# Kernel tuning notes

Hardware: AMD Instinct MI355X
Metric: run time of the kernel (lower is better)

Reference implementation:

```python
import jax, jax.numpy as jnp
import numpy as np

B, S, D, H, E, K, F, FS = 4, 2048, 1024, 16, 8, 2, 4096, 2048
HD = D // H
EPS = 1e-5
T = B * S
CAP = int(1.25 * K * T / E)  # capacity factor 1.25 -> 2560 tokens/expert


def _ln(x, g, b):
    mu = jnp.mean(x, -1, keepdims=True)
    var = jnp.var(x, -1, keepdims=True)
    return (x - mu) * jax.lax.rsqrt(var + EPS) * g + b


def _forward(x, attention_mask, ln1_g, ln1_b, wq, bq, wk, bk, wv, bv, wo, bo,
             ln2_g, ln2_b, w_router, w1, b1, w2, b2, ws1, bs1, ws2, bs2):
    # ---- pre-LN self-attention + residual ----
    xn = _ln(x, ln1_g, ln1_b)
    q = (xn @ wq + bq).reshape(B, S, H, HD)
    k = (xn @ wk + bk).reshape(B, S, H, HD)
    v = (xn @ wv + bv).reshape(B, S, H, HD)
    scores = jnp.einsum('bqhd,bkhd->bhqk', q, k) / np.float32(np.sqrt(HD))
    scores = jnp.where(attention_mask[:, None, None, :], jnp.finfo(scores.dtype).min, scores)
    p = jax.nn.softmax(scores, axis=-1)
    attn = jnp.einsum('bhqk,bkhd->bqhd', p, v).reshape(B, S, D) @ wo + bo
    x = x + attn
    # ---- pre-LN sparse MoE FFN + residual ----
    xn = _ln(x, ln2_g, ln2_b).reshape(T, D)
    logits = xn.astype(jnp.float32) @ w_router              # router in fp32, [T,E]
    probs = jax.nn.softmax(logits, axis=-1)
    topv, topi = jax.lax.top_k(probs, K)                    # [T,K]
    topv = topv / jnp.sum(topv, -1, keepdims=True)          # renormalize top-k gates
    oh = jax.nn.one_hot(topi, E, dtype=jnp.float32)         # [T,K,E]
    flat = oh.transpose(1, 0, 2).reshape(K * T, E)          # slot-major routing priority
    pos_tok = jnp.sum((jnp.cumsum(flat, axis=0) - 1.0) * flat, -1)  # slot position within expert
    keep = pos_tok < CAP                                    # drop tokens over capacity
    posc = jnp.clip(pos_tok, 0, CAP - 1).astype(jnp.int32)
    eidx = topi.T.reshape(K * T)
    w = topv.T.reshape(K * T) * keep
    xt = jnp.tile(xn, (K, 1)) * keep[:, None]               # [K*T, D]
    disp = jnp.zeros((E, CAP, D), xn.dtype).at[eidx, posc].add(xt)   # dispatch [E,C,D]
    h = jax.nn.gelu(jnp.einsum('ecd,edf->ecf', disp, w1) + b1[:, None, :], approximate=False)
    eo = jnp.einsum('ecf,efd->ecd', h, w2) + b2[:, None, :]          # expert out [E,C,D]
    y = jnp.sum(eo[eidx, posc].reshape(K, T, D) * w.reshape(K, T, 1), axis=0)  # combine
    # shared expert (dense, always active)
    y = y + jax.nn.gelu(xn @ ws1 + bs1, approximate=False) @ ws2 + bs2
    return x + y.reshape(B, S, D)


def setup_inputs() -> dict:
    key = jax.random.key(0)
    ks = jax.random.split(key, 16)
    g = lambda k, shape, fan: jax.random.normal(k, shape, jnp.float32) * (fan ** -0.5)
    return {
        'x': jax.random.normal(ks[0], (B, S, D), jnp.float32),
        'attention_mask': jnp.zeros((B, S), bool),
        'ln1_g': jnp.ones((D,), jnp.float32), 'ln1_b': jnp.zeros((D,), jnp.float32),
        'wq': g(ks[1], (D, D), D), 'bq': jnp.zeros((D,), jnp.float32),
        'wk': g(ks[2], (D, D), D), 'bk': jnp.zeros((D,), jnp.float32),
        'wv': g(ks[3], (D, D), D), 'bv': jnp.zeros((D,), jnp.float32),
        'wo': g(ks[4], (D, D), D), 'bo': jnp.zeros((D,), jnp.float32),
        'ln2_g': jnp.ones((D,), jnp.float32), 'ln2_b': jnp.zeros((D,), jnp.float32),
        'w_router': g(ks[5], (D, E), D),
        'w1': g(ks[6], (E, D, F), D), 'b1': jnp.zeros((E, F), jnp.float32),
        'w2': g(ks[7], (E, F, D), F), 'b2': jnp.zeros((E, D), jnp.float32),
        'ws1': g(ks[8], (D, FS), D), 'bs1': jnp.zeros((FS,), jnp.float32),
        'ws2': g(ks[9], (FS, D), FS), 'bs2': jnp.zeros((D,), jnp.float32),
    }


def reference(x, attention_mask, ln1_g, ln1_b, wq, bq, wk, bk, wv, bv, wo, bo,
              ln2_g, ln2_b, w_router, w1, b1, w2, b2, ws1, bs1, ws2, bs2):
    return _forward(x, attention_mask, ln1_g, ln1_b, wq, bq, wk, bk, wv, bv, wo, bo,
                    ln2_g, ln2_b, w_router, w1, b1, w2, b2, ws1, bs1, ws2, bs2)
```

## Files before the change

### kernel.cpp

```cpp
#include <hip/hip_runtime.h>
#include <hip/hip_bf16.h>
#include <stdint.h>

#define D_ 1024
#define S_ 2048
#define B_ 4
#define H_ 16
#define T_ 8192
#define E_ 8
#define CAP_ 2560
#define F_ 4096
#define FS_ 2048

typedef __attribute__((ext_vector_type(8))) short s8v;
typedef __attribute__((ext_vector_type(4))) float f4v;

#define GLL(gp, lp) __builtin_amdgcn_global_load_lds( \
    (const __attribute__((address_space(1))) unsigned int*)(gp), \
    (__attribute__((address_space(3))) unsigned int*)(lp), 16, 0, 0)

__device__ inline short f2bf(float f) {
    union { float f; unsigned u; } v; v.f = f;
    unsigned r = (v.u + 0x7fffu + ((v.u >> 16) & 1u)) >> 16;
    return (short)(r & 0xffffu);
}
__device__ inline float b2f(short h) {
    union { unsigned u; float f; } v; v.u = ((unsigned)(unsigned short)h) << 16; return v.f;
}
__device__ inline float gelu_f(float x) {
    return 0.5f * x * (1.0f + erff(x * 0.7071067811865475f));
}
__device__ inline f4v f4zero() { f4v z; z[0]=0.f; z[1]=0.f; z[2]=0.f; z[3]=0.f; return z; }

__device__ inline unsigned pk2(float a, float b, unsigned* lo) {
    const short ha = f2bf(a), hb = f2bf(b);
    const short la = f2bf(a - b2f(ha)), lb = f2bf(b - b2f(hb));
    *lo = ((unsigned)(unsigned short)lb << 16) | (unsigned)(unsigned short)la;
    return ((unsigned)(unsigned short)hb << 16) | (unsigned)(unsigned short)ha;
}

__global__ __launch_bounds__(256) void transcvt(const float* __restrict__ in,
                                                short* __restrict__ out, int R, int C)
{
    __shared__ float tile[32][33];
    const int tid = threadIdx.x;
    const int tx = tid & 31, ty = tid >> 5;
    const long long ib = (long long)blockIdx.z * R * C;
    const int r0 = blockIdx.y * 32, c0 = blockIdx.x * 32;
#pragma unroll
    for (int i = 0; i < 4; i++)
        tile[ty + i * 8][tx] = in[ib + (long long)(r0 + ty + i * 8) * C + c0 + tx];
    __syncthreads();
#pragma unroll
    for (int i = 0; i < 4; i++)
        out[ib + (long long)(c0 + ty + i * 8) * R + r0 + tx] = f2bf(tile[tx][ty + i * 8]);
}

__global__ __launch_bounds__(256) void transcvt2(const float* __restrict__ in,
    short* __restrict__ oh, short* __restrict__ ol, int R, int C)
{
    __shared__ float tile[32][33];
    const int tid = threadIdx.x;
    const int tx = tid & 31, ty = tid >> 5;
    const int r0 = blockIdx.y * 32, c0 = blockIdx.x * 32;
#pragma unroll
    for (int i = 0; i < 4; i++)
        tile[ty + i * 8][tx] = in[(long long)(r0 + ty + i * 8) * C + c0 + tx];
    __syncthreads();
#pragma unroll
    for (int i = 0; i < 4; i++) {
        const float v = tile[tx][ty + i * 8];
        const short h = f2bf(v);
        const long long o = (long long)(c0 + ty + i * 8) * R + r0 + tx;
        oh[o] = h;
        ol[o] = f2bf(v - b2f(h));
    }
}

__global__ __launch_bounds__(256) void ln1_split(const float* __restrict__ x,
    const float* __restrict__ g, const float* __restrict__ bta,
    short* __restrict__ xh, short* __restrict__ xl)
{
    const int t = blockIdx.x, tid = threadIdx.x;
    const float4 v = ((const float4*)(x + (long long)t * D_))[tid];
    float s1 = v.x + v.y + v.z + v.w;
    float s2 = v.x * v.x + v.y * v.y + v.z * v.z + v.w * v.w;
#pragma unroll
    for (int off = 32; off; off >>= 1) { s1 += __shfl_xor(s1, off, 64); s2 += __shfl_xor(s2, off, 64); }
    __shared__ float r1[4], r2[4];
    if ((tid & 63) == 0) { r1[tid >> 6] = s1; r2[tid >> 6] = s2; }
    __syncthreads();
    s1 = r1[0] + r1[1] + r1[2] + r1[3];
    s2 = r2[0] + r2[1] + r2[2] + r2[3];
    const float mu = s1 * (1.0f / D_);
    const float var = s2 * (1.0f / D_) - mu * mu;
    const float rs = rsqrtf(var + 1e-5f);
    const float4 gv = ((const float4*)g)[tid];
    const float4 bv = ((const float4*)bta)[tid];
    float xn[4];
    xn[0] = (v.x - mu) * rs * gv.x + bv.x;
    xn[1] = (v.y - mu) * rs * gv.y + bv.y;
    xn[2] = (v.z - mu) * rs * gv.z + bv.z;
    xn[3] = (v.w - mu) * rs * gv.w + bv.w;
    short4 hh, ll;
    hh.x = f2bf(xn[0]); ll.x = f2bf(xn[0] - b2f(hh.x));
    hh.y = f2bf(xn[1]); ll.y = f2bf(xn[1] - b2f(hh.y));
    hh.z = f2bf(xn[2]); ll.z = f2bf(xn[2] - b2f(hh.z));
    hh.w = f2bf(xn[3]); ll.w = f2bf(xn[3] - b2f(hh.w));
    ((short4*)(xh + (long long)t * D_))[tid] = hh;
    ((short4*)(xl + (long long)t * D_))[tid] = ll;
}

__global__ __launch_bounds__(256) void ln2_router_kernel(const float* __restrict__ x,
    const float* __restrict__ g, const float* __restrict__ bta, const float* __restrict__ wr,
    short* __restrict__ xo, int* __restrict__ topi, float* __restrict__ gates)
{
    const int t = blockIdx.x, tid = threadIdx.x;
    const float4 v = ((const float4*)(x + (long long)t * D_))[tid];
    float s1 = v.x + v.y + v.z + v.w;
    float s2 = v.x * v.x + v.y * v.y + v.z * v.z + v.w * v.w;
#pragma unroll
    for (int off = 32; off; off >>= 1) { s1 += __shfl_xor(s1, off, 64); s2 += __shfl_xor(s2, off, 64); }
    __shared__ float r1[4], r2[4];
    if ((tid & 63) == 0) { r1[tid >> 6] = s1; r2[tid >> 6] = s2; }
    __syncthreads();
    s1 = r1[0] + r1[1] + r1[2] + r1[3];
    s2 = r2[0] + r2[1] + r2[2] + r2[3];
    const float mu = s1 * (1.0f / D_);
    const float var = s2 * (1.0f / D_) - mu * mu;
    const float rs = rsqrtf(var + 1e-5f);
    const float4 gv = ((const float4*)g)[tid];
    const float4 bv = ((const float4*)bta)[tid];
    float xn[4];
    xn[0] = (v.x - mu) * rs * gv.x + bv.x;
    xn[1] = (v.y - mu) * rs * gv.y + bv.y;
    xn[2] = (v.z - mu) * rs * gv.z + bv.z;
    xn[3] = (v.w - mu) * rs * gv.w + bv.w;
    short4 o;
    o.x = f2bf(xn[0]); o.y = f2bf(xn[1]); o.z = f2bf(xn[2]); o.w = f2bf(xn[3]);
    ((short4*)(xo + (long long)t * D_))[tid] = o;

    float a8[8] = {0, 0, 0, 0, 0, 0, 0, 0};
#pragma unroll
    for (int q = 0; q < 4; q++) {
        const int d = tid * 4 + q;
        const float4 w0 = ((const float4*)(wr + d * 8))[0];
        const float4 w1 = ((const float4*)(wr + d * 8))[1];
        a8[0] += xn[q] * w0.x; a8[1] += xn[q] * w0.y; a8[2] += xn[q] * w0.z; a8[3] += xn[q] * w0.w;
        a8[4] += xn[q] * w1.x; a8[5] += xn[q] * w1.y; a8[6] += xn[q] * w1.z; a8[7] += xn[q] * w1.w;
    }
    __shared__ float lred[32];
#pragma unroll
    for (int e = 0; e < 8; e++) {
        float vv = a8[e];
#pragma unroll
        for (int off = 32; off; off >>= 1) vv += __shfl_xor(vv, off, 64);
        if ((tid & 63) == 0) lred[(tid >> 6) * 8 + e] = vv;
    }
    __syncthreads();
    if (tid == 0) {
        float lg[8];
#pragma unroll
        for (int e = 0; e < 8; e++) lg[e] = lred[e] + lred[8 + e] + lred[16 + e] + lred[24 + e];
        int e0 = 0;
        for (int e = 1; e < 8; e++) if (lg[e] > lg[e0]) e0 = e;
        int e1 = (e0 == 0) ? 1 : 0;
        for (int e = 0; e < 8; e++) if (e != e0 && lg[e] > lg[e1]) e1 = e;
        const float mx = lg[e0];
        float den = 0.f;
        for (int e = 0; e < 8; e++) den += expf(lg[e] - mx);
        const float p0 = expf(lg[e0] - mx) / den;
        const float p1 = expf(lg[e1] - mx) / den;
        const float inv = 1.0f / (p0 + p1);
        topi[t * 2] = e0; topi[t * 2 + 1] = e1;
        gates[t * 2] = p0 * inv; gates[t * 2 + 1] = p1 * inv;
    }
}

__global__ __launch_bounds__(256) void route_scan(const int* __restrict__ topi,
    const float* __restrict__ gates, int* __restrict__ posc, float* __restrict__ wv)
{
    const int tid = threadIdx.x;
    const int w = tid >> 6, lane = tid & 63;
    __shared__ int wsum[4 * 8];
    int cnt[8] = {0, 0, 0, 0, 0, 0, 0, 0};
    const int base_r = tid * 64;
    for (int i = 0; i < 64; i++) {
        const int r = base_r + i;
        const int k = r >> 13, t = r & (T_ - 1);
        cnt[topi[t * 2 + k]]++;
    }
    int excl[8];
#pragma unroll
    for (int e = 0; e < 8; e++) {
        int x = cnt[e];
#pragma unroll
        for (int off = 1; off < 64; off <<= 1) {
            int y = __shfl_up(x, off, 64);
            if (lane >= off) x += y;
        }
        excl[e] = x - cnt[e];
        if (lane == 63) wsum[w * 8 + e] = x;
    }
    __syncthreads();
    int pos[8];
#pragma unroll
    for (int e = 0; e < 8; e++) {
        int s = 0;
        for (int ww = 0; ww < 4; ww++) if (ww < w) s += wsum[ww * 8 + e];
        pos[e] = s + excl[e];
    }
    for (int i = 0; i < 64; i++) {
        const int r = base_r + i;
        const int k = r >> 13, t = r & (T_ - 1);
        const int e = topi[t * 2 + k];
        const int p = pos[e]++;
        const bool keep = p < CAP_;
        posc[r] = keep ? p : -1;
        wv[r] = keep ? gates[t * 2 + k] : 0.0f;
    }
}

__global__ __launch_bounds__(128) void dispatch_kernel(const short* __restrict__ xn2,
    const int* __restrict__ topi, const int* __restrict__ posc, short* __restrict__ disp)
{
    const int r = blockIdx.x;
    const int p = posc[r];
    if (p < 0) return;
    const int k = r >> 13, t = r & (T_ - 1);
    const int e = topi[t * 2 + k];
    const int tid = threadIdx.x;
    *(s8v*)&disp[((long long)e * CAP_ + p) * D_ + tid * 8] =
        *(const s8v*)&xn2[(long long)t * D_ + tid * 8];
}

__global__ __launch_bounds__(256) void combine_kernel(const float* __restrict__ x1,
    const float* __restrict__ ys, const float* __restrict__ eo,
    const int* __restrict__ topi, const int* __restrict__ posc,
    const float* __restrict__ wv, float* __restrict__ out)
{
    const int t = blockIdx.x, tid = threadIdx.x;
    float4 a = *(const float4*)&x1[(long long)t * D_ + tid * 4];
    const float4 b = *(const float4*)&ys[(long long)t * D_ + tid * 4];
    a.x += b.x; a.y += b.y; a.z += b.z; a.w += b.w;
#pragma unroll
    for (int k = 0; k < 2; k++) {
        const int r = k * T_ + t;
        const int p = posc[r];
        if (p >= 0) {
            const int e = topi[t * 2 + k];
            const float wt = wv[r];
            const float4 c = *(const float4*)&eo[((long long)e * CAP_ + p) * D_ + tid * 4];
            a.x += wt * c.x; a.y += wt * c.y; a.z += wt * c.z; a.w += wt * c.w;
        }
    }
    *(float4*)&out[(long long)t * D_ + tid * 4] = a;
}

template <int EPI>
__global__ __launch_bounds__(256) void gemm_btz(
    const short* __restrict__ A, const short* __restrict__ Bt,
    const float* __restrict__ bias, void* __restrict__ Cout,
    int M, int N, int K, int ldc,
    long long sA, long long sB, long long sBias, long long sC)
{
    __shared__ __align__(16) short lA[128 * 32];
    __shared__ __align__(16) short lB[128 * 32];
    const int z = blockIdx.z;
    A += (long long)z * sA;
    Bt += (long long)z * sB;
    bias += (long long)z * sBias;
    const int tid = threadIdx.x;
    const int wvi = tid >> 6, lane = tid & 63, lid = lane & 15, quad = lane >> 4;
    const int wm = wvi >> 1, wn = wvi & 1;
    const int mBase = blockIdx.y * 128, nBase = blockIdx.x * 128;
    f4v acc[4][4];
#pragma unroll
    for (int i = 0; i < 4; i++)
#pragma unroll
        for (int j = 0; j < 4; j++) acc[i][j] = f4zero();
    const long long aOff0 = (long long)(mBase + (tid >> 2)) * K + (tid & 3) * 8;
    const long long aOff1 = aOff0 + 64LL * K;
    const long long bOff0 = (long long)(nBase + (tid >> 2)) * K + (tid & 3) * 8;
    const long long bOff1 = bOff0 + 64LL * K;
    const int wofs = wvi << 9;
    for (int k0 = 0; k0 < K; k0 += 32) {
        __syncthreads();
        GLL(A + aOff0 + k0, &lA[wofs]);  GLL(A + aOff1 + k0, &lA[2048 + wofs]);
        GLL(Bt + bOff0 + k0, &lB[wofs]); GLL(Bt + bOff1 + k0, &lB[2048 + wofs]);
        __syncthreads();
        s8v af[4], bf[4];
#pragma unroll
        for (int i = 0; i < 4; i++)
            af[i] = *(const s8v*)&lA[(wm * 64 + i * 16 + lid) * 32 + quad * 8];
#pragma unroll
        for (int j = 0; j < 4; j++)
            bf[j] = *(const s8v*)&lB[(wn * 64 + j * 16 + lid) * 32 + quad * 8];
#pragma unroll
        for (int i = 0; i < 4; i++)
#pragma unroll
            for (int j = 0; j < 4; j++)
                acc[i][j] = __builtin_amdgcn_mfma_f32_16x16x32_bf16(af[i], bf[j], acc[i][j], 0, 0, 0);
    }
    const int mW = mBase + wm * 64 + quad * 4;
    const int nW = nBase + wn * 64 + lid;
    short* Cs = (short*)Cout + (long long)z * sC;
    float* Cf = (float*)Cout + (long long)z * sC;
#pragma unroll
    for (int j = 0; j < 4; j++) {
        const int n = nW + j * 16;
        const float bn = bias[n];
#pragma unroll
        for (int i = 0; i < 4; i++) {
            const int m = mW + i * 16;
#pragma unroll
            for (int r = 0; r < 4; r++) {
                float v = acc[i][j][r] + bn;
                if (EPI == 1) { v = gelu_f(v); Cs[(long long)(m + r) * ldc + n] = f2bf(v); }
                else          { Cf[(long long)(m + r) * ldc + n] = v; }
            }
        }
    }
}

template <int EPI>
__global__ __launch_bounds__(256) void gemm_hl(
    const short* __restrict__ Ah, const short* __restrict__ Al,
    const short* __restrict__ Bh, const short* __restrict__ Bl,
    const float* __restrict__ biasQ, const float* __restrict__ biasK,
    const float* __restrict__ biasV, const float* __restrict__ resid,
    short* __restrict__ Ch, short* __restrict__ Cl, float* __restrict__ Cf,
    int M, int N, int K, int ldc)
{
    __shared__ __align__(16) short lAh[4096], lAl[4096], lBh[4096], lBl[4096];
    const int tid = threadIdx.x;
    const int wvi = tid >> 6, lane = tid & 63, lid = lane & 15, quad = lane >> 4;
    const int wm = wvi >> 1, wn = wvi & 1;
    const int mBase = blockIdx.y * 128, nBase = blockIdx.x * 128;
    f4v acc[4][4];
#pragma unroll
    for (int i = 0; i < 4; i++)
#pragma unroll
        for (int j = 0; j < 4; j++) acc[i][j] = f4zero();
    const long long aOff0 = (long long)(mBase + (tid >> 2)) * K + (tid & 3) * 8;
    const long long aOff1 = aOff0 + 64LL * K;
    const long long bOff0 = (long long)(nBase + (tid >> 2)) * K + (tid & 3) * 8;
    const long long bOff1 = bOff0 + 64LL * K;
    const int wofs = wvi << 9;
    for (int k0 = 0; k0 < K; k0 += 32) {
        __syncthreads();
        GLL(Ah + aOff0 + k0, &lAh[wofs]);  GLL(Ah + aOff1 + k0, &lAh[2048 + wofs]);
        GLL(Al + aOff0 + k0, &lAl[wofs]);  GLL(Al + aOff1 + k0, &lAl[2048 + wofs]);
        GLL(Bh + bOff0 + k0, &lBh[wofs]);  GLL(Bh + bOff1 + k0, &lBh[2048 + wofs]);
        GLL(Bl + bOff0 + k0, &lBl[wofs]);  GLL(Bl + bOff1 + k0, &lBl[2048 + wofs]);
        __syncthreads();
        s8v ah[4], al[4], bh[4], bl[4];
#pragma unroll
        for (int i = 0; i < 4; i++) {
            const int ro = (wm * 64 + i * 16 + lid) * 32 + quad * 8;
            ah[i] = *(const s8v*)&lAh[ro];
            al[i] = *(const s8v*)&lAl[ro];
        }
#pragma unroll
        for (int j = 0; j < 4; j++) {
            const int ro = (wn * 64 + j * 16 + lid) * 32 + quad * 8;
            bh[j] = *(const s8v*)&lBh[ro];
            bl[j] = *(const s8v*)&lBl[ro];
        }
#pragma unroll
        for (int i = 0; i < 4; i++)
#pragma unroll
            for (int j = 0; j < 4; j++) {
                acc[i][j] = __builtin_amdgcn_mfma_f32_16x16x32_bf16(ah[i], bh[j], acc[i][j], 0, 0, 0);
                acc[i][j] = __builtin_amdgcn_mfma_f32_16x16x32_bf16(ah[i], bl[j], acc[i][j], 0, 0, 0);
                acc[i][j] = __builtin_amdgcn_mfma_f32_16x16x32_bf16(al[i], bh[j], acc[i][j], 0, 0, 0);
            }
    }
    const int mW = mBase + wm * 64 + quad * 4;
    const int nW = nBase + wn * 64 + lid;
#pragma unroll
    for (int j = 0; j < 4; j++) {
        const int n = nW + j * 16;
        const float* bp = (n < 1024) ? biasQ : ((n < 2048) ? biasK : biasV);
        const float bn = bp[n & 1023];
#pragma unroll
        for (int i = 0; i < 4; i++) {
            const int m = mW + i * 16;
#pragma unroll
            for (int r = 0; r < 4; r++) {
                const float v = acc[i][j][r] + bn;
                const long long o = (long long)(m + r) * ldc + n;
                if (EPI == 0) {
                    const short h = f2bf(v);
                    Ch[o] = h;
                    Cl[o] = f2bf(v - b2f(h));
                } else {
                    Cf[o] = v + resid[o];
                }
            }
        }
    }
}

__global__ __launch_bounds__(256) void flash_attn_hl(const short* __restrict__ qkvh,
    const short* __restrict__ qkvl, const unsigned char* __restrict__ mask,
    short* __restrict__ attnh, short* __restrict__ attnl)
{
    __shared__ __align__(16) short lKh[32 * 72], lKl[32 * 72];
    __shared__ __align__(16) short lVth[64 * 40], lVtl[64 * 40];
    const int tid = threadIdx.x;
    const int lane = tid & 63, lid = lane & 15, quad = lane >> 4;
    const int w = tid >> 6;
    const int bh = blockIdx.y;
    const int b = bh >> 4, h = bh & 15;
    const int q0row = blockIdx.x * 64 + w * 16;

    const long long rowQ = (long long)(b * S_ + q0row + lid) * 3072 + h * 64;
    const s8v qh0 = *(const s8v*)&qkvh[rowQ + quad * 8];
    const s8v qh1 = *(const s8v*)&qkvh[rowQ + 32 + quad * 8];
    const s8v ql0 = *(const s8v*)&qkvl[rowQ + quad * 8];
    const s8v ql1 = *(const s8v*)&qkvl[rowQ + 32 + quad * 8];

    float m_run = -1e30f, l_run = 0.0f;
    f4v o[4];
#pragma unroll
    for (int dt = 0; dt < 4; dt++) o[dt] = f4zero();

    const unsigned char* mrow = mask + b * S_;
    const int srow = tid >> 3, sgrp = tid & 7;
    const int srcA = lid + ((quad & 1) << 5);
    const int srcB = srcA + 16;

    for (int c0 = 0; c0 < S_; c0 += 32) {
        __syncthreads();
        {
            const long long gk = (long long)(b * S_ + c0 + srow) * 3072 + 1024 + h * 64 + sgrp * 8;
            *(s8v*)&lKh[srow * 72 + sgrp * 8] = *(const s8v*)&qkvh[gk];
            *(s8v*)&lKl[srow * 72 + sgrp * 8] = *(const s8v*)&qkvl[gk];
            const long long gv = (long long)(b * S_ + c0 + srow) * 3072 + 2048 + h * 64 + sgrp * 8;
            const s8v vh = *(const s8v*)&qkvh[gv];
            const s8v vl = *(const s8v*)&qkvl[gv];
            const int vcol = srow ^ ((sgrp & 3) << 3);
#pragma unroll
            for (int jj = 0; jj < 8; jj++) {
                lVth[(sgrp * 8 + jj) * 40 + vcol] = vh[jj];
                lVtl[(sgrp * 8 + jj) * 40 + vcol] = vl[jj];
            }
        }
        __syncthreads();

        f4v s0 = f4zero(), s1 = f4zero();
        {
            const int r0 = lid * 72 + quad * 8;
            const s8v kh0a = *(const s8v*)&lKh[r0];
            const s8v kh0b = *(const s8v*)&lKh[r0 + 32];
            const s8v kl0a = *(const s8v*)&lKl[r0];
            const s8v kl0b = *(const s8v*)&lKl[r0 + 32];
            s0 = __builtin_amdgcn_mfma_f32_16x16x32_bf16(kh0a, qh0, s0, 0, 0, 0);
            s0 = __builtin_amdgcn_mfma_f32_16x16x32_bf16(kh0b, qh1, s0, 0, 0, 0);
            s0 = __builtin_amdgcn_mfma_f32_16x16x32_bf16(kl0a, qh0, s0, 0, 0, 0);
            s0 = __builtin_amdgcn_mfma_f32_16x16x32_bf16(kl0b, qh1, s0, 0, 0, 0);
            s0 = __builtin_amdgcn_mfma_f32_16x16x32_bf16(kh0a, ql0, s0, 0, 0, 0);
            s0 = __builtin_amdgcn_mfma_f32_16x16x32_bf16(kh0b, ql1, s0, 0, 0, 0);
            const int r1i = (16 + lid) * 72 + quad * 8;
            const s8v kh1a = *(const s8v*)&lKh[r1i];
            const s8v kh1b = *(const s8v*)&lKh[r1i + 32];
            const s8v kl1a = *(const s8v*)&lKl[r1i];
            const s8v kl1b = *(const s8v*)&lKl[r1i + 32];
            s1 = __builtin_amdgcn_mfma_f32_16x16x32_bf16(kh1a, qh0, s1, 0, 0, 0);
            s1 = __builtin_amdgcn_mfma_f32_16x16x32_bf16(kh1b, qh1, s1, 0, 0, 0);
            s1 = __builtin_amdgcn_mfma_f32_16x16x32_bf16(kl1a, qh0, s1, 0, 0, 0);
            s1 = __builtin_amdgcn_mfma_f32_16x16x32_bf16(kl1b, qh1, s1, 0, 0, 0);
            s1 = __builtin_amdgcn_mfma_f32_16x16x32_bf16(kh1a, ql0, s1, 0, 0, 0);
            s1 = __builtin_amdgcn_mfma_f32_16x16x32_bf16(kh1b, ql1, s1, 0, 0, 0);
        }
        const unsigned mm0 = *(const unsigned*)(mrow + c0 + quad * 4);
        const unsigned mm1 = *(const unsigned*)(mrow + c0 + 16 + quad * 4);
        float p[8];
#pragma unroll
        for (int r = 0; r < 4; r++) {
            p[r]     = ((mm0 >> (8 * r)) & 255u) ? -1e30f : s0[r] * 0.125f;
            p[4 + r] = ((mm1 >> (8 * r)) & 255u) ? -1e30f : s1[r] * 0.125f;
        }
        float mx = fmaxf(fmaxf(fmaxf(p[0], p[1]), fmaxf(p[2], p[3])),
                         fmaxf(fmaxf(p[4], p[5]), fmaxf(p[6], p[7])));
        mx = fmaxf(mx, __shfl_xor(mx, 16, 64));
        mx = fmaxf(mx, __shfl_xor(mx, 32, 64));
        const float mn = fmaxf(m_run, mx);
        const float alpha = __expf(m_run - mn);
        m_run = mn;
        float rs = 0.0f;
#pragma unroll
        for (int i = 0; i < 8; i++) { p[i] = __expf(p[i] - mn); rs += p[i]; }
        rs += __shfl_xor(rs, 16, 64);
        rs += __shfl_xor(rs, 32, 64);
        l_run = l_run * alpha + rs;
#pragma unroll
        for (int dt = 0; dt < 4; dt++)
#pragma unroll
            for (int r = 0; r < 4; r++) o[dt][r] *= alpha;

        unsigned c0l, c1l, c2l, c3l;
        const unsigned c0h = pk2(p[0], p[1], &c0l);
        const unsigned c1h = pk2(p[2], p[3], &c1l);
        const unsigned c2h = pk2(p[4], p[5], &c2l);
        const unsigned c3h = pk2(p[6], p[7], &c3l);
        union { s8v v; unsigned u[4]; } pah, pal;
        {
            const unsigned a0 = __shfl((int)c0h, srcA, 64), a2 = __shfl((int)c2h, srcA, 64);
            const unsigned a1 = __shfl((int)c1h, srcA, 64), a3 = __shfl((int)c3h, srcA, 64);
            const unsigned b0 = __shfl((int)c0h, srcB, 64), b2 = __shfl((int)c2h, srcB, 64);
            const unsigned b1 = __shfl((int)c1h, srcB, 64), b3 = __shfl((int)c3h, srcB, 64);
            const bool lo = (quad < 2);
            pah.u[0] = lo ? a0 : a2; pah.u[1] = lo ? a1 : a3;
            pah.u[2] = lo ? b0 : b2; pah.u[3] = lo ? b1 : b3;
        }
        {
            const unsigned a0 = __shfl((int)c0l, srcA, 64), a2 = __shfl((int)c2l, srcA, 64);
            const unsigned a1 = __shfl((int)c1l, srcA, 64), a3 = __shfl((int)c3l, srcA, 64);
            const unsigned b0 = __shfl((int)c0l, srcB, 64), b2 = __shfl((int)c2l, srcB, 64);
            const unsigned b1 = __shfl((int)c1l, srcB, 64), b3 = __shfl((int)c3l, srcB, 64);
            const bool lo = (quad < 2);
            pal.u[0] = lo ? a0 : a2; pal.u[1] = lo ? a1 : a3;
            pal.u[2] = lo ? b0 : b2; pal.u[3] = lo ? b1 : b3;
        }

#pragma unroll
        for (int dt = 0; dt < 4; dt++) {
            const int d = dt * 16 + lid;
            const int x3 = (dt * 2 + (lid >> 3)) & 3;
            const int ro = d * 40 + ((quad ^ x3) << 3);
            const s8v bvh = *(const s8v*)&lVth[ro];
            const s8v bvl = *(const s8v*)&lVtl[ro];
            o[dt] = __builtin_amdgcn_mfma_f32_16x16x32_bf16(bvh, pah.v, o[dt], 0, 0, 0);
            o[dt] = __builtin_amdgcn_mfma_f32_16x16x32_bf16(bvl, pah.v, o[dt], 0, 0, 0);
            o[dt] = __builtin_amdgcn_mfma_f32_16x16x32_bf16(bvh, pal.v, o[dt], 0, 0, 0);
        }
    }
    const float inv_l = 1.0f / l_run;
    const long long obase = (long long)(b * S_ + q0row + lid) * D_ + h * 64 + quad * 4;
#pragma unroll
    for (int dt = 0; dt < 4; dt++) {
        short4 hh4, ll4;
        float v0 = o[dt][0] * inv_l, v1 = o[dt][1] * inv_l;
        float v2 = o[dt][2] * inv_l, v3 = o[dt][3] * inv_l;
        hh4.x = f2bf(v0); ll4.x = f2bf(v0 - b2f(hh4.x));
        hh4.y = f2bf(v1); ll4.y = f2bf(v1 - b2f(hh4.y));
        hh4.z = f2bf(v2); ll4.z = f2bf(v2 - b2f(hh4.z));
        hh4.w = f2bf(v3); ll4.w = f2bf(v3 - b2f(hh4.w));
        *(short4*)&attnh[obase + dt * 16] = hh4;
        *(short4*)&attnl[obase + dt * 16] = ll4;
    }
}

constexpr long long SZ_DD2   = (long long)D_ * D_ * 2;
constexpr long long OFF_WQKVH = 0;
constexpr long long OFF_WQKVL = OFF_WQKVH + 3 * SZ_DD2;
constexpr long long OFF_WOH   = OFF_WQKVL + 3 * SZ_DD2;
constexpr long long OFF_WOL   = OFF_WOH + SZ_DD2;
constexpr long long OFF_W1T   = OFF_WOL + SZ_DD2;
constexpr long long OFF_W2T   = OFF_W1T + (long long)E_ * F_ * D_ * 2;
constexpr long long OFF_WS1T  = OFF_W2T + (long long)E_ * D_ * F_ * 2;
constexpr long long OFF_WS2T  = OFF_WS1T + (long long)FS_ * D_ * 2;
constexpr long long OFF_X1    = OFF_WS2T + (long long)D_ * FS_ * 2;
constexpr long long OFF_XN2   = OFF_X1 + (long long)T_ * D_ * 4;
constexpr long long OFF_TOPI  = OFF_XN2 + (long long)T_ * D_ * 2;
constexpr long long OFF_GATES = OFF_TOPI + (long long)T_ * 2 * 4;
constexpr long long OFF_POSC  = OFF_GATES + (long long)T_ * 2 * 4;
constexpr long long OFF_WVAL  = OFF_POSC + (long long)2 * T_ * 4;
constexpr long long ZONE      = OFF_WVAL + (long long)2 * T_ * 4;
constexpr long long OFF_XH1   = ZONE;
constexpr long long OFF_XL1   = OFF_XH1 + (long long)T_ * D_ * 2;
constexpr long long OFF_QKVH  = OFF_XL1 + (long long)T_ * D_ * 2;
constexpr long long OFF_QKVL  = OFF_QKVH + (long long)T_ * 3 * D_ * 2;
constexpr long long OFF_ATTNH = OFF_QKVL + (long long)T_ * 3 * D_ * 2;
constexpr long long OFF_ATTNL = OFF_ATTNH + (long long)T_ * D_ * 2;
constexpr long long OFF_DISP  = ZONE;
constexpr long long OFF_H     = OFF_DISP + (long long)E_ * CAP_ * D_ * 2;
constexpr long long OFF_EO    = OFF_H + (long long)4 * CAP_ * F_ * 2;
constexpr long long OFF_YS    = OFF_EO + (long long)E_ * CAP_ * D_ * 4;
constexpr long long OFF_HS    = ZONE;

extern "C" void kernel_launch(void* const* d_in, const int* in_sizes, int n_in,
                              void* d_out, int out_size, void* d_ws, size_t ws_size,
                              hipStream_t stream)
{
    (void)in_sizes; (void)n_in; (void)out_size; (void)ws_size;
    const float* x       = (const float*)d_in[0];
    const unsigned char* mask = (const unsigned char*)d_in[1];
    const float* ln1g    = (const float*)d_in[2];
    const float* ln1b    = (const float*)d_in[3];
    const float* wq      = (const float*)d_in[4];
    const float* bq      = (const float*)d_in[5];
    const float* wk      = (const float*)d_in[6];
    const float* bk      = (const float*)d_in[7];
    const float* wvp     = (const float*)d_in[8];
    const float* bvv     = (const float*)d_in[9];
    const float* wo      = (const float*)d_in[10];
    const float* bo      = (const float*)d_in[11];
    const float* ln2g    = (const float*)d_in[12];
    const float* ln2b    = (const float*)d_in[13];
    const float* wrouter = (const float*)d_in[14];
    const float* w1      = (const float*)d_in[15];
    const float* b1      = (const float*)d_in[16];
    const float* w2      = (const float*)d_in[17];
    const float* b2      = (const float*)d_in[18];
    const float* ws1     = (const float*)d_in[19];
    const float* bs1     = (const float*)d_in[20];
    const float* ws2     = (const float*)d_in[21];
    const float* bs2     = (const float*)d_in[22];
    float* out = (float*)d_out;
    char* ws = (char*)d_ws;

    short* wqkvh = (short*)(ws + OFF_WQKVH);
    short* wqkvl = (short*)(ws + OFF_WQKVL);
    short* woh   = (short*)(ws + OFF_WOH);
    short* wol   = (short*)(ws + OFF_WOL);
    short* w1T   = (short*)(ws + OFF_W1T);
    short* w2T   = (short*)(ws + OFF_W2T);
    short* ws1T  = (short*)(ws + OFF_WS1T);
    short* ws2T  = (short*)(ws + OFF_WS2T);
    float* x1    = (float*)(ws + OFF_X1);
    short* xn2   = (short*)(ws + OFF_XN2);
    int*   topi  = (int*)(ws + OFF_TOPI);
    float* gates = (float*)(ws + OFF_GATES);
    int*   posc  = (int*)(ws + OFF_POSC);
    float* wval  = (float*)(ws + OFF_WVAL);
    short* xh1   = (short*)(ws + OFF_XH1);
    short* xl1   = (short*)(ws + OFF_XL1);
    short* qkvh  = (short*)(ws + OFF_QKVH);
    short* qkvl  = (short*)(ws + OFF_QKVL);
    short* attnh = (short*)(ws + OFF_ATTNH);
    short* attnl = (short*)(ws + OFF_ATTNL);
    short* disp  = (short*)(ws + OFF_DISP);
    short* hbuf  = (short*)(ws + OFF_H);
    float* eo    = (float*)(ws + OFF_EO);
    short* hs    = (short*)(ws + OFF_HS);
    float* ysb   = (float*)(ws + OFF_YS);

    const dim3 tb(256);
    transcvt2<<<dim3(32, 32), tb, 0, stream>>>(wq,  wqkvh,               wqkvl,               1024, 1024);
    transcvt2<<<dim3(32, 32), tb, 0, stream>>>(wk,  wqkvh + 1024 * 1024, wqkvl + 1024 * 1024, 1024, 1024);
    transcvt2<<<dim3(32, 32), tb, 0, stream>>>(wvp, wqkvh + 2 * 1024 * 1024, wqkvl + 2 * 1024 * 1024, 1024, 1024);
    transcvt2<<<dim3(32, 32), tb, 0, stream>>>(wo,  woh, wol, 1024, 1024);
    transcvt<<<dim3(128, 32, 8), tb, 0, stream>>>(w1, w1T, 1024, 4096);
    transcvt<<<dim3(32, 128, 8), tb, 0, stream>>>(w2, w2T, 4096, 1024);
    transcvt<<<dim3(64, 32, 1), tb, 0, stream>>>(ws1, ws1T, 1024, 2048);
    transcvt<<<dim3(32, 64, 1), tb, 0, stream>>>(ws2, ws2T, 2048, 1024);

    ln1_split<<<T_, 256, 0, stream>>>(x, ln1g, ln1b, xh1, xl1);

    gemm_hl<0><<<dim3(24, 64), 256, 0, stream>>>(xh1, xl1, wqkvh, wqkvl,
        bq, bk, bvv, nullptr, qkvh, qkvl, nullptr, T_, 3072, 1024, 3072);

    flash_attn_hl<<<dim3(32, 64), 256, 0, stream>>>(qkvh, qkvl, mask, attnh, attnl);

    gemm_hl<1><<<dim3(8, 64), 256, 0, stream>>>(attnh, attnl, woh, wol,
        bo, bo, bo, x, nullptr, nullptr, x1, T_, 1024, 1024, 1024);

    ln2_router_kernel<<<T_, 256, 0, stream>>>(x1, ln2g, ln2b, wrouter, xn2, topi, gates);
    route_scan<<<1, 256, 0, stream>>>(topi, gates, posc, wval);
    dispatch_kernel<<<2 * T_, 128, 0, stream>>>(xn2, topi, posc, disp);

    for (int g = 0; g < 2; g++) {
        const long long e0 = (long long)g * 4;
        gemm_btz<1><<<dim3(32, 20, 4), 256, 0, stream>>>(
            disp + e0 * CAP_ * D_, w1T + e0 * F_ * D_, b1 + e0 * F_, hbuf,
            CAP_, F_, 1024, F_,
            (long long)CAP_ * D_, (long long)F_ * D_, (long long)F_, (long long)CAP_ * F_);
        gemm_btz<2><<<dim3(8, 20, 4), 256, 0, stream>>>(
            hbuf, w2T + e0 * D_ * F_, b2 + e0 * D_, eo + e0 * CAP_ * D_,
            CAP_, 1024, F_, 1024,
            (long long)CAP_ * F_, (long long)D_ * F_, (long long)D_, (long long)CAP_ * D_);
    }

    gemm_btz<1><<<dim3(16, 64, 1), 256, 0, stream>>>(xn2, ws1T, bs1, hs,
        T_, FS_, 1024, FS_, 0, 0, 0, 0);
    gemm_btz<2><<<dim3(8, 64, 1), 256, 0, stream>>>(hs, ws2T, bs2, ysb,
        T_, 1024, FS_, 1024, 0, 0, 0, 0);

    combine_kernel<<<T_, 256, 0, stream>>>(x1, ysb, eo, topi, posc, wval, out);
}
```

Baseline: 1.928 ms.

## Prefetch K/V tiles into registers, add lazy softmax rescale and MFMA priority

The flash-attention inner loop now loads the next 32-row K/V chunk from global memory into registers right after the LDS barrier, so the load overlaps the current chunk's MFMAs. The online softmax skips the max update and the rescale of the accumulator whenever the new chunk max stays within 8 of the running max across the wavefront. s_setprio is raised around the MFMA blocks to favour matrix issue. The cost is extra register pressure, and the skipped rescale lets exp values grow up to e^8, which relies on fp32 headroom.

```diff
diff --git a/kernel.cpp b/kernel.cpp
--- a/kernel.cpp
+++ b/kernel.cpp
@@ -428,26 +428,38 @@
 
     const unsigned char* mrow = mask + b * S_;
     const int srow = tid >> 3, sgrp = tid & 7;
+    const int vcol = srow ^ ((sgrp & 3) << 3);
     const int srcA = lid + ((quad & 1) << 5);
     const int srcB = srcA + 16;
+
+    s8v kh_r, kl_r, vh_r, vl_r;
+    {
+        const long long gk = (long long)(b * S_ + srow) * 3072 + 1024 + h * 64 + sgrp * 8;
+        kh_r = *(const s8v*)&qkvh[gk];
+        kl_r = *(const s8v*)&qkvl[gk];
+        vh_r = *(const s8v*)&qkvh[gk + 1024];
+        vl_r = *(const s8v*)&qkvl[gk + 1024];
+    }
 
     for (int c0 = 0; c0 < S_; c0 += 32) {
         __syncthreads();
         {
-            const long long gk = (long long)(b * S_ + c0 + srow) * 3072 + 1024 + h * 64 + sgrp * 8;
-            *(s8v*)&lKh[srow * 72 + sgrp * 8] = *(const s8v*)&qkvh[gk];
-            *(s8v*)&lKl[srow * 72 + sgrp * 8] = *(const s8v*)&qkvl[gk];
-            const long long gv = (long long)(b * S_ + c0 + srow) * 3072 + 2048 + h * 64 + sgrp * 8;
-            const s8v vh = *(const s8v*)&qkvh[gv];
-            const s8v vl = *(const s8v*)&qkvl[gv];
-            const int vcol = srow ^ ((sgrp & 3) << 3);
+            *(s8v*)&lKh[srow * 72 + sgrp * 8] = kh_r;
+            *(s8v*)&lKl[srow * 72 + sgrp * 8] = kl_r;
 #pragma unroll
             for (int jj = 0; jj < 8; jj++) {
-                lVth[(sgrp * 8 + jj) * 40 + vcol] = vh[jj];
-                lVtl[(sgrp * 8 + jj) * 40 + vcol] = vl[jj];
+                lVth[(sgrp * 8 + jj) * 40 + vcol] = vh_r[jj];
+                lVtl[(sgrp * 8 + jj) * 40 + vcol] = vl_r[jj];
             }
         }
         __syncthreads();
+        if (c0 + 32 < S_) {
+            const long long gk = (long long)(b * S_ + c0 + 32 + srow) * 3072 + 1024 + h * 64 + sgrp * 8;
+            kh_r = *(const s8v*)&qkvh[gk];
+            kl_r = *(const s8v*)&qkvl[gk];
+            vh_r = *(const s8v*)&qkvh[gk + 1024];
+            vl_r = *(const s8v*)&qkvl[gk + 1024];
+        }
 
         f4v s0 = f4zero(), s1 = f4zero();
         {
@@ -456,23 +468,25 @@
             const s8v kh0b = *(const s8v*)&lKh[r0 + 32];
             const s8v kl0a = *(const s8v*)&lKl[r0];
             const s8v kl0b = *(const s8v*)&lKl[r0 + 32];
+            const int r1i = (16 + lid) * 72 + quad * 8;
+            const s8v kh1a = *(const s8v*)&lKh[r1i];
+            const s8v kh1b = *(const s8v*)&lKh[r1i + 32];
+            const s8v kl1a = *(const s8v*)&lKl[r1i];
+            const s8v kl1b = *(const s8v*)&lKl[r1i + 32];
+            __builtin_amdgcn_s_setprio(1);
             s0 = __builtin_amdgcn_mfma_f32_16x16x32_bf16(kh0a, qh0, s0, 0, 0, 0);
             s0 = __builtin_amdgcn_mfma_f32_16x16x32_bf16(kh0b, qh1, s0, 0, 0, 0);
             s0 = __builtin_amdgcn_mfma_f32_16x16x32_bf16(kl0a, qh0, s0, 0, 0, 0);
             s0 = __builtin_amdgcn_mfma_f32_16x16x32_bf16(kl0b, qh1, s0, 0, 0, 0);
             s0 = __builtin_amdgcn_mfma_f32_16x16x32_bf16(kh0a, ql0, s0, 0, 0, 0);
             s0 = __builtin_amdgcn_mfma_f32_16x16x32_bf16(kh0b, ql1, s0, 0, 0, 0);
-            const int r1i = (16 + lid) * 72 + quad * 8;
-            const s8v kh1a = *(const s8v*)&lKh[r1i];
-            const s8v kh1b = *(const s8v*)&lKh[r1i + 32];
-            const s8v kl1a = *(const s8v*)&lKl[r1i];
-            const s8v kl1b = *(const s8v*)&lKl[r1i + 32];
             s1 = __builtin_amdgcn_mfma_f32_16x16x32_bf16(kh1a, qh0, s1, 0, 0, 0);
             s1 = __builtin_amdgcn_mfma_f32_16x16x32_bf16(kh1b, qh1, s1, 0, 0, 0);
             s1 = __builtin_amdgcn_mfma_f32_16x16x32_bf16(kl1a, qh0, s1, 0, 0, 0);
             s1 = __builtin_amdgcn_mfma_f32_16x16x32_bf16(kl1b, qh1, s1, 0, 0, 0);
             s1 = __builtin_amdgcn_mfma_f32_16x16x32_bf16(kh1a, ql0, s1, 0, 0, 0);
             s1 = __builtin_amdgcn_mfma_f32_16x16x32_bf16(kh1b, ql1, s1, 0, 0, 0);
+            __builtin_amdgcn_s_setprio(0);
         }
         const unsigned mm0 = *(const unsigned*)(mrow + c0 + quad * 4);
         const unsigned mm1 = *(const unsigned*)(mrow + c0 + 16 + quad * 4);
@@ -486,19 +500,28 @@
                          fmaxf(fmaxf(p[4], p[5]), fmaxf(p[6], p[7])));
         mx = fmaxf(mx, __shfl_xor(mx, 16, 64));
         mx = fmaxf(mx, __shfl_xor(mx, 32, 64));
-        const float mn = fmaxf(m_run, mx);
-        const float alpha = __expf(m_run - mn);
-        m_run = mn;
-        float rs = 0.0f;
-#pragma unroll
-        for (int i = 0; i < 8; i++) { p[i] = __expf(p[i] - mn); rs += p[i]; }
-        rs += __shfl_xor(rs, 16, 64);
-        rs += __shfl_xor(rs, 32, 64);
-        l_run = l_run * alpha + rs;
-#pragma unroll
-        for (int dt = 0; dt < 4; dt++)
-#pragma unroll
-            for (int r = 0; r < 4; r++) o[dt][r] *= alpha;
+        if (__all(mx - m_run <= 8.0f)) {
+            float rs = 0.0f;
+#pragma unroll
+            for (int i = 0; i < 8; i++) { p[i] = __expf(p[i] - m_run); rs += p[i]; }
+            rs += __shfl_xor(rs, 16, 64);
+            rs += __shfl_xor(rs, 32, 64);
+            l_run += rs;
+        } else {
+            const float mn = fmaxf(m_run, mx);
+            const float alpha = __expf(m_run - mn);
+            m_run = mn;
+            float rs = 0.0f;
+#pragma unroll
+            for (int i = 0; i < 8; i++) { p[i] = __expf(p[i] - mn); rs += p[i]; }
+            rs += __shfl_xor(rs, 16, 64);
+            rs += __shfl_xor(rs, 32, 64);
+            l_run = l_run * alpha + rs;
+#pragma unroll
+            for (int dt = 0; dt < 4; dt++)
+#pragma unroll
+                for (int r = 0; r < 4; r++) o[dt][r] *= alpha;
+        }
 
         unsigned c0l, c1l, c2l, c3l;
         const unsigned c0h = pk2(p[0], p[1], &c0l);
@@ -525,6 +548,7 @@
             pal.u[2] = lo ? b0 : b2; pal.u[3] = lo ? b1 : b3;
         }
 
+        __builtin_amdgcn_s_setprio(1);
 #pragma unroll
         for (int dt = 0; dt < 4; dt++) {
             const int d = dt * 16 + lid;
@@ -536,6 +560,7 @@
             o[dt] = __builtin_amdgcn_mfma_f32_16x16x32_bf16(bvl, pah.v, o[dt], 0, 0, 0);
             o[dt] = __builtin_amdgcn_mfma_f32_16x16x32_bf16(bvh, pal.v, o[dt], 0, 0, 0);
         }
+        __builtin_amdgcn_s_setprio(0);
     }
     const float inv_l = 1.0f / l_run;
     const long long obase = (long long)(b * S_ + q0row + lid) * D_ + h * 64 + quad * 4;
```

Result: no change. 1.891 ms (-1.9%).
